# Performance work log

Measured on AMD Instinct MI355X. Metric: run time of the kernel, lower is better.

The kernel has to match this reference:

```python
import jax, jax.numpy as jnp
import numpy as np
from jax import lax

DIM = 128
HEADS = 8
HEAD_DIM = DIM // HEADS
SR = 2
B, H, W = 2, 80, 80
SCALE = HEAD_DIM ** (-0.5)
BN_EPS = 1e-5


def _conv1x1(x, w, b):
    # x: (B,C,H,W), w: (O,C), b: (O,)
    return jnp.einsum('bchw,oc->bohw', x, w) + b[None, :, None, None]


def setup_inputs() -> dict:
    key = jax.random.key(0)
    ks = jax.random.split(key, 12)
    s = DIM ** -0.5
    x = jax.random.normal(ks[0], (B, DIM, H, W), dtype=jnp.float32)
    q_w = jax.random.normal(ks[1], (DIM, DIM), dtype=jnp.float32) * s
    q_b = jnp.zeros((DIM,), jnp.float32)
    k_w = jax.random.normal(ks[2], (DIM, DIM), dtype=jnp.float32) * s
    k_b = jnp.zeros((DIM,), jnp.float32)
    v_w = jax.random.normal(ks[3], (DIM, DIM), dtype=jnp.float32) * s
    v_b = jnp.zeros((DIM,), jnp.float32)
    sr_w = jax.random.normal(ks[4], (DIM, DIM, SR, SR), dtype=jnp.float32) * (s / SR)
    sr_b = jnp.zeros((DIM,), jnp.float32)
    bn_gamma = jnp.ones((DIM,), jnp.float32)
    bn_beta = jnp.zeros((DIM,), jnp.float32)
    bn_mean = jnp.zeros((DIM,), jnp.float32)
    bn_var = jnp.ones((DIM,), jnp.float32)
    proj_w = jax.random.normal(ks[5], (DIM, DIM), dtype=jnp.float32) * s
    proj_b = jnp.zeros((DIM,), jnp.float32)
    return dict(x=x, q_w=q_w, q_b=q_b, k_w=k_w, k_b=k_b, v_w=v_w, v_b=v_b,
                sr_w=sr_w, sr_b=sr_b, bn_gamma=bn_gamma, bn_beta=bn_beta,
                bn_mean=bn_mean, bn_var=bn_var, proj_w=proj_w, proj_b=proj_b)


def reference(x, q_w, q_b, k_w, k_b, v_w, v_b, sr_w, sr_b,
              bn_gamma, bn_beta, bn_mean, bn_var, proj_w, proj_b):
    b, c, h, w = x.shape
    n = h * w
    # q: (B,h,N,d)
    q = _conv1x1(x, q_w, q_b).reshape(b, HEADS, HEAD_DIM, n).transpose(0, 1, 3, 2)
    # spatial reduction: Conv2d(k=SR, s=SR) + BN(eval) + ReLU
    x_kv = lax.conv_general_dilated(x, sr_w, window_strides=(SR, SR),
                                    padding='VALID',
                                    dimension_numbers=('NCHW', 'OIHW', 'NCHW'))
    x_kv = x_kv + sr_b[None, :, None, None]
    inv = bn_gamma / jnp.sqrt(bn_var + BN_EPS)
    x_kv = x_kv * inv[None, :, None, None] + (bn_beta - bn_mean * inv)[None, :, None, None]
    x_kv = jax.nn.relu(x_kv)
    n_kv = x_kv.shape[2] * x_kv.shape[3]
    k = _conv1x1(x_kv, k_w, k_b).reshape(b, HEADS, HEAD_DIM, n_kv).transpose(0, 1, 3, 2)
    v = _conv1x1(x_kv, v_w, v_b).reshape(b, HEADS, HEAD_DIM, n_kv).transpose(0, 1, 3, 2)
    # explicit attention: (B,h,N,N_kv)
    attn = jnp.einsum('bhnd,bhmd->bhnm', q, k) * SCALE
    attn = jax.nn.softmax(attn, axis=-1)
    out = jnp.einsum('bhnm,bhmd->bhnd', attn, v)  # (B,h,N,d)
    # faithful to source layout: transpose(1,2) then reshape to (B,C,H,W)
    out = out.transpose(0, 2, 1, 3).reshape(b, c, h, w)
    out = _conv1x1(out, proj_w, proj_b)
    return out
```

## Files before the change

kernel.cpp:

```cpp
#include <hip/hip_runtime.h>
#include <hip/hip_bf16.h>
#include <cmath>

#define DIM 128
#define HEADS 8
#define NBATCH 2
#define NQ 6400
#define NKV 1600
#define NC 50
#define BN_EPS 1e-5f
#define LOG2E 1.4426950408889634f

typedef __bf16 bf16_t;
typedef __attribute__((ext_vector_type(8))) __bf16 bf16x8;
typedef __attribute__((ext_vector_type(16))) float f32x16;

union BF8U { bf16x8 v; unsigned u[4]; };

__device__ inline unsigned packbf2(float a, float b) {
  union { __hip_bfloat162 v; unsigned u; } r;
  r.v = __float22bfloat162_rn(make_float2(a, b));
  return r.u;
}

__device__ inline unsigned short f2bf(float v) {
  unsigned u = __float_as_uint(v);
  return (unsigned short)((u + 0x7FFFu + ((u >> 16) & 1u)) >> 16);
}

__global__ __launch_bounds__(256) void prep_all(
    const float* __restrict__ x,
    const float* __restrict__ qw, const float* __restrict__ kw,
    const float* __restrict__ vw, const float* __restrict__ pw,
    const float* __restrict__ srw,
    unsigned short* __restrict__ Xb,
    unsigned short* __restrict__ Wb,
    unsigned short* __restrict__ X4b,
    unsigned short* __restrict__ Vp)
{
  int t = threadIdx.x;
  int bx = blockIdx.x;
  if (bx < 1600) {
    __shared__ float tile[32][33];
    int tx = t & 31, ty = t >> 5;
    int b = bx / 800;
    int rem = bx % 800;
    int c0 = (rem / 200) * 32, s0 = (rem % 200) * 32;
#pragma unroll
    for (int r = 0; r < 32; r += 8)
      tile[ty + r][tx] = x[((size_t)b * DIM + c0 + ty + r) * NQ + s0 + tx];
    __syncthreads();
#pragma unroll
    for (int r = 0; r < 32; r += 8)
      Xb[((size_t)b * NQ + s0 + ty + r) * DIM + c0 + tx] = f2bf(tile[tx][ty + r]);
    return;
  }
  if (bx < 2240) {
    __shared__ float itile[16][164];
    int idx0 = bx - 1600;
    int b  = idx0 / 320;
    int rem = idx0 % 320;
    int i  = rem / 8;
    int c0 = (rem % 8) * 16;
    const float* xb = x + ((size_t)b * DIM + c0) * NQ + (size_t)i * 160;
#pragma unroll
    for (int k = 0; k < 10; ++k) {
      int idx = t + k * 256;
      int r = idx / 160, col = idx % 160;
      itile[r][col] = xb[(size_t)r * NQ + col];
    }
    __syncthreads();
    unsigned short* ob = X4b + ((size_t)b * NKV + (size_t)i * 40) * 512 + c0 * 4;
#pragma unroll
    for (int k = 0; k < 10; ++k) {
      int idx = t + k * 256;
      int j = idx >> 6, cc = idx & 63;
      int cr = cc >> 2, ky = (cc >> 1) & 1, kx = cc & 1;
      ob[(size_t)j * 512 + cc] = f2bf(itile[cr][ky * 80 + 2 * j + kx]);
    }
    return;
  }
  int e = (bx - 2240) * 256 + t;
  if (e < 131072) {
    const float* src; int idx;
    if (e < 16384)      { src = qw;  idx = e; }
    else if (e < 32768) { src = kw;  idx = e - 16384; }
    else if (e < 49152) { src = vw;  idx = e - 32768; }
    else if (e < 65536) { src = pw;  idx = e - 49152; }
    else                { src = srw; idx = e - 65536; }
    Wb[e] = f2bf(src[idx]);
  }
  if (e < NBATCH * HEADS * NC * 32) {
    int cid = e >> 5;
    int pos = e & 31;
    size_t addr = (size_t)cid * 1024 + 256 + ((pos & 16) ? 512 : 0) + (pos & 15);
    Vp[addr] = 0x3F80;
  }
}

__global__ __launch_bounds__(256) void mgemm_qsrkv(
    const bf16_t* __restrict__ Xb, const bf16_t* __restrict__ X4b,
    const bf16_t* __restrict__ Wb,
    const float* __restrict__ q_b, const float* __restrict__ sr_b,
    const float* __restrict__ k_b, const float* __restrict__ v_b,
    const float* __restrict__ bng, const float* __restrict__ bnb,
    const float* __restrict__ bnm, const float* __restrict__ bnv,
    unsigned short* __restrict__ Qb,
    unsigned short* __restrict__ Kp, unsigned short* __restrict__ Vp,
    float sl)
{
  __shared__ __align__(16) unsigned short xs[32][136];
  int t = threadIdx.x;
  int ln = t & 31, hf = (t >> 5) & 1, wid = t >> 6;
  int b = blockIdx.y;
  int o = wid * 32 + ln;

  if (blockIdx.x < 50) {
    int s0 = blockIdx.x * 32;
    const bf16_t* arow = &X4b[((size_t)b * NKV + s0 + ln) * 512 + hf * 8];
    const bf16_t* brow = &Wb[65536 + (size_t)o * 512 + hf * 8];
    f32x16 acc = {};
#pragma unroll 8
    for (int c0 = 0; c0 < 512; c0 += 16) {
      bf16x8 af = *(const bf16x8*)&arow[c0];
      bf16x8 bf = *(const bf16x8*)&brow[c0];
      acc = __builtin_amdgcn_mfma_f32_32x32x16_bf16(af, bf, acc, 0, 0, 0);
    }
    float bv = sr_b[o];
    float inv = bng[o] / sqrtf(bnv[o] + BN_EPS);
    float b2 = bnb[o] - bnm[o] * inv;
#pragma unroll
    for (int g = 0; g < 4; ++g)
#pragma unroll
      for (int j = 0; j < 4; ++j) {
        int s = 8 * g + 4 * hf + j;
        xs[s][o] = f2bf(fmaxf((acc[4 * g + j] + bv) * inv + b2, 0.f));
      }
    __syncthreads();

    const unsigned short* ar2 = &xs[ln][hf * 8];
    const bf16_t* kbrow = &Wb[16384 + (size_t)o * DIM + hf * 8];
    const bf16_t* vbrow = &Wb[32768 + (size_t)o * DIM + hf * 8];
    f32x16 ka = {}, va = {};
#pragma unroll
    for (int c0 = 0; c0 < 128; c0 += 16) {
      bf16x8 af = *(const bf16x8*)&ar2[c0];
      bf16x8 kb = *(const bf16x8*)&kbrow[c0];
      bf16x8 vb = *(const bf16x8*)&vbrow[c0];
      ka = __builtin_amdgcn_mfma_f32_32x32x16_bf16(af, kb, ka, 0, 0, 0);
      va = __builtin_amdgcn_mfma_f32_32x32x16_bf16(af, vb, va, 0, 0, 0);
    }
    int hloc = o >> 4, d = o & 15;
    {
      float kb2 = k_b[o];
      size_t CB = (((size_t)b * HEADS + hloc) * NC + (s0 >> 5)) * 512;
#pragma unroll
      for (int g = 0; g < 4; ++g)
#pragma unroll
        for (int j = 0; j < 4; ++j) {
          int sl2 = 8 * g + 4 * hf + j;
          Kp[CB + sl2 * 16 + d] = f2bf(ka[4 * g + j] + kb2);
        }
    }
    {
      float vb2 = v_b[o];
      size_t CB = (((size_t)b * HEADS + hloc) * NC + (s0 >> 5)) * 1024;
      uint4 w0, w1;
      w0.x = packbf2(va[0] + vb2, va[1] + vb2);
      w0.y = packbf2(va[2] + vb2, va[3] + vb2);
      w0.z = packbf2(va[4] + vb2, va[5] + vb2);
      w0.w = packbf2(va[6] + vb2, va[7] + vb2);
      w1.x = packbf2(va[8] + vb2, va[9] + vb2);
      w1.y = packbf2(va[10] + vb2, va[11] + vb2);
      w1.z = packbf2(va[12] + vb2, va[13] + vb2);
      w1.w = packbf2(va[14] + vb2, va[15] + vb2);
      *(uint4*)&Vp[CB + d * 16 + hf * 8] = w0;
      *(uint4*)&Vp[CB + 512 + d * 16 + hf * 8] = w1;
    }
  } else {
    int s0 = (blockIdx.x - 50) * 32;
    const bf16_t* arow = &Xb[((size_t)b * NQ + s0 + ln) * DIM + hf * 8];
    const bf16_t* brow = &Wb[(size_t)o * DIM + hf * 8];
    f32x16 acc = {};
#pragma unroll
    for (int c0 = 0; c0 < 128; c0 += 16) {
      bf16x8 af = *(const bf16x8*)&arow[c0];
      bf16x8 bf = *(const bf16x8*)&brow[c0];
      acc = __builtin_amdgcn_mfma_f32_32x32x16_bf16(af, bf, acc, 0, 0, 0);
    }
    float bv = q_b[o];
#pragma unroll
    for (int g = 0; g < 4; ++g)
#pragma unroll
      for (int j = 0; j < 4; ++j) {
        int s = s0 + 8 * g + 4 * hf + j;
        Qb[((size_t)b * NQ + s) * DIM + o] = f2bf((acc[4 * g + j] + bv) * sl);
      }
  }
}

__global__ __launch_bounds__(256) void attn_split(
    const bf16_t* __restrict__ Qb, const bf16_t* __restrict__ Kp,
    const bf16_t* __restrict__ Vp, unsigned short* __restrict__ Pb,
    float* __restrict__ Lsum)
{
  const int t = threadIdx.x;
  const int ln = t & 31, hf = (t >> 5) & 1, wid = t >> 6;
  const int h = blockIdx.y;
  const int b = blockIdx.z & 1, half = blockIdx.z >> 1;
  const int q0 = blockIdx.x * 128 + wid * 32;

  bf16x8 qf = *(const bf16x8*)&Qb[((size_t)b * NQ + q0 + ln) * DIM + h * 16 + hf * 8];
  const int bh = b * HEADS + h;
  const bf16_t* kc = &Kp[((size_t)bh * NC + half * 25) * 512 + ln * 16 + hf * 8];
  const bf16_t* vc = &Vp[((size_t)bh * NC + half * 25) * 1024 + ln * 16 + hf * 8];

  f32x16 acc0 = {}, acc1 = {};
  const f32x16 zero = {};

  bf16x8 kf0 = *(const bf16x8*)kc;
  bf16x8 va0 = *(const bf16x8*)vc;
  bf16x8 vb0 = *(const bf16x8*)(vc + 512);
  bf16x8 kf1 = *(const bf16x8*)(kc + 512);
  bf16x8 va1 = *(const bf16x8*)(vc + 1024);
  bf16x8 vb1 = *(const bf16x8*)(vc + 1536);

  f32x16 S0 = __builtin_amdgcn_mfma_f32_32x32x16_bf16(kf0, qf, zero, 0, 0, 0);

  for (int c = 0; c < 25; ++c) {
    int cn = (c + 2 < 25) ? c + 2 : 24;
    bf16x8 kf2 = *(const bf16x8*)(kc + (size_t)cn * 512);
    bf16x8 va2 = *(const bf16x8*)(vc + (size_t)cn * 1024);
    bf16x8 vb2 = *(const bf16x8*)(vc + (size_t)cn * 1024 + 512);

    f32x16 S1 = __builtin_amdgcn_mfma_f32_32x32x16_bf16(kf1, qf, zero, 0, 0, 0);

    BF8U f0, f1;
#pragma unroll
    for (int i = 0; i < 4; ++i) {
      f0.u[i] = packbf2(__builtin_amdgcn_exp2f(S0[2 * i]),
                        __builtin_amdgcn_exp2f(S0[2 * i + 1]));
      f1.u[i] = packbf2(__builtin_amdgcn_exp2f(S0[8 + 2 * i]),
                        __builtin_amdgcn_exp2f(S0[9 + 2 * i]));
    }

    acc0 = __builtin_amdgcn_mfma_f32_32x32x16_bf16(va0, f0.v, acc0, 0, 0, 0);
    acc1 = __builtin_amdgcn_mfma_f32_32x32x16_bf16(vb0, f1.v, acc1, 0, 0, 0);

    S0 = S1;
    kf0 = kf1; va0 = va1; vb0 = vb1;
    kf1 = kf2; va1 = va2; vb1 = vb2;
  }

  f32x16 acc;
#pragma unroll
  for (int i = 0; i < 16; ++i) acc[i] = acc0[i] + acc1[i];

  unsigned short* prow =
      &Pb[(size_t)(half * 2 + b) * (NQ * DIM) + (size_t)(q0 + ln) * DIM + h * 16 + 4 * hf];
  uint2 w0, w1;
  w0.x = packbf2(acc[0], acc[1]); w0.y = packbf2(acc[2], acc[3]);
  w1.x = packbf2(acc[4], acc[5]); w1.y = packbf2(acc[6], acc[7]);
  *(uint2*)&prow[0] = w0;
  *(uint2*)&prow[8] = w1;
  if (!hf)
    Lsum[(size_t)(half * 2 + b) * (HEADS * NQ) + (size_t)h * NQ + q0 + ln] = acc[8];
}

__global__ __launch_bounds__(256) void proj_comb(
    const unsigned short* __restrict__ Pb, const float* __restrict__ Lsum,
    const bf16_t* __restrict__ Wb, const float* __restrict__ p_b,
    float* __restrict__ Out)
{
  __shared__ __align__(16) unsigned short As[32][136];
  int t = threadIdx.x;
  int b = blockIdx.y;
  int s0 = blockIdx.x * 32;

  {
    int tx = t & 31, cg = t >> 5;
#pragma unroll
    for (int it = 0; it < 16; ++it) {
      int c = cg * 16 + it;
      int f = c * NQ + s0 + tx;
      int n = f >> 7, hh = (f >> 4) & 7;
      float p0 = __uint_as_float((unsigned)Pb[(size_t)b * (NQ * DIM) + f] << 16);
      float p1 = __uint_as_float((unsigned)Pb[(size_t)(2 + b) * (NQ * DIM) + f] << 16);
      float L = Lsum[(size_t)b * (HEADS * NQ) + (size_t)hh * NQ + n] +
                Lsum[(size_t)(2 + b) * (HEADS * NQ) + (size_t)hh * NQ + n];
      As[tx][c] = f2bf((p0 + p1) / L);
    }
  }
  __syncthreads();

  int ln = t & 31, hf = (t >> 5) & 1, wid = t >> 6;
  int o = wid * 32 + ln;
  const bf16_t* brow = &Wb[49152 + (size_t)o * DIM + hf * 8];
  const unsigned short* arow = &As[ln][hf * 8];
  f32x16 acc = {};
#pragma unroll
  for (int c0 = 0; c0 < 128; c0 += 16) {
    bf16x8 af = *(const bf16x8*)&arow[c0];
    bf16x8 bf = *(const bf16x8*)&brow[c0];
    acc = __builtin_amdgcn_mfma_f32_32x32x16_bf16(af, bf, acc, 0, 0, 0);
  }
  float bv = p_b[o];
  float* obase = &Out[((size_t)b * DIM + o) * NQ + s0 + 4 * hf];
#pragma unroll
  for (int g = 0; g < 4; ++g) {
    float4 r;
    r.x = acc[4 * g + 0] + bv; r.y = acc[4 * g + 1] + bv;
    r.z = acc[4 * g + 2] + bv; r.w = acc[4 * g + 3] + bv;
    *(float4*)&obase[8 * g] = r;
  }
}

extern "C" void kernel_launch(void* const* d_in, const int* in_sizes, int n_in,
                              void* d_out, int out_size, void* d_ws, size_t ws_size,
                              hipStream_t stream)
{
  const float* x    = (const float*)d_in[0];
  const float* q_w  = (const float*)d_in[1];
  const float* q_b  = (const float*)d_in[2];
  const float* k_w  = (const float*)d_in[3];
  const float* k_b  = (const float*)d_in[4];
  const float* v_w  = (const float*)d_in[5];
  const float* v_b  = (const float*)d_in[6];
  const float* sr_w = (const float*)d_in[7];
  const float* sr_b = (const float*)d_in[8];
  const float* bng  = (const float*)d_in[9];
  const float* bnb  = (const float*)d_in[10];
  const float* bnm  = (const float*)d_in[11];
  const float* bnv  = (const float*)d_in[12];
  const float* p_w  = (const float*)d_in[13];
  const float* p_b  = (const float*)d_in[14];
  float* out = (float*)d_out;

  float* ws = (float*)d_ws;
  bf16_t* Xb   = (bf16_t*)(ws);
  bf16_t* X4b  = (bf16_t*)(ws + 819200);
  bf16_t* Qb   = (bf16_t*)(ws + 1638400);
  bf16_t* Kp   = (bf16_t*)(ws + 2457600);
  bf16_t* Vp   = (bf16_t*)(ws + 2662400);
  float*  Lsum = ws + 3072000;
  bf16_t* Wb   = (bf16_t*)(ws + 3276800);
  bf16_t* Pb   = (bf16_t*)(ws + 3342336);

  const float sl = 0.25f * LOG2E;

  prep_all<<<dim3(2880), dim3(256), 0, stream>>>(
      x, q_w, k_w, v_w, p_w, sr_w,
      (unsigned short*)Xb, (unsigned short*)Wb,
      (unsigned short*)X4b, (unsigned short*)Vp);

  mgemm_qsrkv<<<dim3(250, NBATCH), dim3(256), 0, stream>>>(
      Xb, X4b, Wb, q_b, sr_b, k_b, v_b, bng, bnb, bnm, bnv,
      (unsigned short*)Qb, (unsigned short*)Kp, (unsigned short*)Vp, sl);

  attn_split<<<dim3(NQ / 128, HEADS, 4), dim3(256), 0, stream>>>(
      Qb, Kp, Vp, (unsigned short*)Pb, Lsum);

  proj_comb<<<dim3(200, NBATCH), dim3(256), 0, stream>>>(
      (const unsigned short*)Pb, Lsum, Wb, p_b, out);
}
```

Baseline: 152.6 us.

## Split attention KV range four ways and stage K/V chunks in shared memory

The attention kernel now splits the 50 KV chunks into four quarters instead of two, doubling the grid, and each block first copies its K/V quarter into LDS before the MFMA loop reads from shared memory. The combine step in the projection kernel sums four partial outputs and four row sums. This aims to raise occupancy/parallelism and cut redundant global K/V reads across the four waves of a block. In exchange it adds a sync and an LDS fill per block, and it doubles the partial-output traffic written and read by the projection kernel. The workspace is relaid to make room.

```diff
diff --git a/kernel.cpp b/kernel.cpp
--- a/kernel.cpp
+++ b/kernel.cpp
@@ -204,34 +204,49 @@
     const bf16_t* __restrict__ Vp, unsigned short* __restrict__ Pb,
     float* __restrict__ Lsum)
 {
+  __shared__ __align__(16) unsigned short kv[13 * 512 + 13 * 1024];
   const int t = threadIdx.x;
   const int ln = t & 31, hf = (t >> 5) & 1, wid = t >> 6;
   const int h = blockIdx.y;
-  const int b = blockIdx.z & 1, half = blockIdx.z >> 1;
+  const int b = blockIdx.z & 1, quarter = blockIdx.z >> 1;
   const int q0 = blockIdx.x * 128 + wid * 32;
-
+  const int kcnt = 12 + (quarter < 2 ? 1 : 0);
+  const int kstart = quarter * 12 + (quarter < 2 ? quarter : 2);
+  const int slice = quarter * 2 + b;
+  const int bh = b * HEADS + h;
+
+  {
+    const uint4* gk = (const uint4*)(Kp + ((size_t)bh * NC + kstart) * 512);
+    const uint4* gv = (const uint4*)(Vp + ((size_t)bh * NC + kstart) * 1024);
+    uint4* lk = (uint4*)kv;
+    uint4* lv = (uint4*)(kv + 13 * 512);
+    int nk = kcnt * 64, nv = kcnt * 128;
+    for (int i = t; i < nk; i += 256) lk[i] = gk[i];
+    for (int i = t; i < nv; i += 256) lv[i] = gv[i];
+  }
   bf16x8 qf = *(const bf16x8*)&Qb[((size_t)b * NQ + q0 + ln) * DIM + h * 16 + hf * 8];
-  const int bh = b * HEADS + h;
-  const bf16_t* kc = &Kp[((size_t)bh * NC + half * 25) * 512 + ln * 16 + hf * 8];
-  const bf16_t* vc = &Vp[((size_t)bh * NC + half * 25) * 1024 + ln * 16 + hf * 8];
+  __syncthreads();
+
+  const unsigned short* kbase = kv + ln * 16 + hf * 8;
+  const unsigned short* vbase = kv + 13 * 512 + ln * 16 + hf * 8;
 
   f32x16 acc0 = {}, acc1 = {};
   const f32x16 zero = {};
 
-  bf16x8 kf0 = *(const bf16x8*)kc;
-  bf16x8 va0 = *(const bf16x8*)vc;
-  bf16x8 vb0 = *(const bf16x8*)(vc + 512);
-  bf16x8 kf1 = *(const bf16x8*)(kc + 512);
-  bf16x8 va1 = *(const bf16x8*)(vc + 1024);
-  bf16x8 vb1 = *(const bf16x8*)(vc + 1536);
+  bf16x8 kf0 = *(const bf16x8*)kbase;
+  bf16x8 va0 = *(const bf16x8*)vbase;
+  bf16x8 vb0 = *(const bf16x8*)(vbase + 512);
+  bf16x8 kf1 = *(const bf16x8*)(kbase + 512);
+  bf16x8 va1 = *(const bf16x8*)(vbase + 1024);
+  bf16x8 vb1 = *(const bf16x8*)(vbase + 1536);
 
   f32x16 S0 = __builtin_amdgcn_mfma_f32_32x32x16_bf16(kf0, qf, zero, 0, 0, 0);
 
-  for (int c = 0; c < 25; ++c) {
-    int cn = (c + 2 < 25) ? c + 2 : 24;
-    bf16x8 kf2 = *(const bf16x8*)(kc + (size_t)cn * 512);
-    bf16x8 va2 = *(const bf16x8*)(vc + (size_t)cn * 1024);
-    bf16x8 vb2 = *(const bf16x8*)(vc + (size_t)cn * 1024 + 512);
+  for (int c = 0; c < kcnt; ++c) {
+    int cn = (c + 2 < kcnt) ? c + 2 : kcnt - 1;
+    bf16x8 kf2 = *(const bf16x8*)(kbase + (size_t)cn * 512);
+    bf16x8 va2 = *(const bf16x8*)(vbase + (size_t)cn * 1024);
+    bf16x8 vb2 = *(const bf16x8*)(vbase + (size_t)cn * 1024 + 512);
 
     f32x16 S1 = __builtin_amdgcn_mfma_f32_32x32x16_bf16(kf1, qf, zero, 0, 0, 0);
 
@@ -257,14 +272,14 @@
   for (int i = 0; i < 16; ++i) acc[i] = acc0[i] + acc1[i];
 
   unsigned short* prow =
-      &Pb[(size_t)(half * 2 + b) * (NQ * DIM) + (size_t)(q0 + ln) * DIM + h * 16 + 4 * hf];
+      &Pb[(size_t)slice * (NQ * DIM) + (size_t)(q0 + ln) * DIM + h * 16 + 4 * hf];
   uint2 w0, w1;
   w0.x = packbf2(acc[0], acc[1]); w0.y = packbf2(acc[2], acc[3]);
   w1.x = packbf2(acc[4], acc[5]); w1.y = packbf2(acc[6], acc[7]);
   *(uint2*)&prow[0] = w0;
   *(uint2*)&prow[8] = w1;
   if (!hf)
-    Lsum[(size_t)(half * 2 + b) * (HEADS * NQ) + (size_t)h * NQ + q0 + ln] = acc[8];
+    Lsum[(size_t)slice * (HEADS * NQ) + (size_t)h * NQ + q0 + ln] = acc[8];
 }
 
 __global__ __launch_bounds__(256) void proj_comb(
@@ -284,11 +299,14 @@
       int c = cg * 16 + it;
       int f = c * NQ + s0 + tx;
       int n = f >> 7, hh = (f >> 4) & 7;
-      float p0 = __uint_as_float((unsigned)Pb[(size_t)b * (NQ * DIM) + f] << 16);
-      float p1 = __uint_as_float((unsigned)Pb[(size_t)(2 + b) * (NQ * DIM) + f] << 16);
-      float L = Lsum[(size_t)b * (HEADS * NQ) + (size_t)hh * NQ + n] +
-                Lsum[(size_t)(2 + b) * (HEADS * NQ) + (size_t)hh * NQ + n];
-      As[tx][c] = f2bf((p0 + p1) / L);
+      float ps = 0.f, L = 0.f;
+#pragma unroll
+      for (int qq = 0; qq < 4; ++qq) {
+        int sl2 = qq * 2 + b;
+        ps += __uint_as_float((unsigned)Pb[(size_t)sl2 * (NQ * DIM) + f] << 16);
+        L += Lsum[(size_t)sl2 * (HEADS * NQ) + (size_t)hh * NQ + n];
+      }
+      As[tx][c] = f2bf(ps / L);
     }
   }
   __syncthreads();
@@ -343,8 +361,8 @@
   bf16_t* Kp   = (bf16_t*)(ws + 2457600);
   bf16_t* Vp   = (bf16_t*)(ws + 2662400);
   float*  Lsum = ws + 3072000;
-  bf16_t* Wb   = (bf16_t*)(ws + 3276800);
-  bf16_t* Pb   = (bf16_t*)(ws + 3342336);
+  bf16_t* Wb   = (bf16_t*)(ws + 3481600);
+  bf16_t* Pb   = (bf16_t*)(ws + 3547136);
 
   const float sl = 0.25f * LOG2E;
 
@@ -357,7 +375,7 @@
       Xb, X4b, Wb, q_b, sr_b, k_b, v_b, bng, bnb, bnm, bnv,
       (unsigned short*)Qb, (unsigned short*)Kp, (unsigned short*)Vp, sl);
 
-  attn_split<<<dim3(NQ / 128, HEADS, 4), dim3(256), 0, stream>>>(
+  attn_split<<<dim3(NQ / 128, HEADS, 8), dim3(256), 0, stream>>>(
       Qb, Kp, Vp, (unsigned short*)Pb, Lsum);
 
   proj_comb<<<dim3(200, NBATCH), dim3(256), 0, stream>>>(
```

Result: no change. 154.2 us (+1.1%).
